# Performance work log

Hardware: AMD Instinct MI355X
Metric: run time of the kernel (lower is better)

## Reference

```python
import jax, jax.numpy as jnp
import numpy as np

TEMPERATURE = 0.07
EPS = 1e-6  # arccosh domain clamp: argument must be >= 1


def setup_inputs() -> dict:
    key = jax.random.key(0)
    k1, k2 = jax.random.split(key)
    N, D = 8192, 768
    v_hyp = jax.random.normal(k1, (N, D), dtype=jnp.float32)
    t_hyp = jax.random.normal(k2, (N, D), dtype=jnp.float32)
    c = jnp.float32(1.0)  # curvature (positive scalar)
    return {"v_hyp": v_hyp, "t_hyp": t_hyp, "c": c}


def _pairwise_hyperbolic_dist(v, t, c):
    # Lorentz/hyperboloid pairwise distance with curvature c:
    #   x_time = sqrt(1/c + ||x||^2)
    #   <x,y>_L = x . y - x_time * y_time
    #   d(x,y) = (1/sqrt(c)) * arccosh(clamp(-c * <x,y>_L, min=1+eps))
    inv_c = 1.0 / c
    v_time = jnp.sqrt(inv_c + jnp.sum(v * v, axis=-1))  # [N]
    t_time = jnp.sqrt(inv_c + jnp.sum(t * t, axis=-1))  # [N]
    lorentz = jnp.einsum("nd,md->nm", v, t) - v_time[:, None] * t_time[None, :]
    arg = jnp.maximum(-c * lorentz, 1.0 + EPS)
    return jnp.sqrt(inv_c) * jnp.arccosh(arg)  # [N, N]


def _ce_diag(logits):
    # cross-entropy with labels = arange(N), mean reduction
    logp = jax.nn.log_softmax(logits, axis=-1)
    return -jnp.mean(jnp.diagonal(logp))


def reference(v_hyp, t_hyp, c):
    dist = _pairwise_hyperbolic_dist(v_hyp, t_hyp, c)
    logits = -dist / TEMPERATURE  # [N, N]
    loss_v2t = _ce_diag(logits)
    loss_t2v = _ce_diag(logits.T)
    return (loss_v2t + loss_t2v) * 0.5
```

## Files before the change

### kernel.cpp

```cpp
#include <hip/hip_runtime.h>
#include <hip/hip_bf16.h>
#include <math.h>

#define NROWS 8192
#define DDIM  768
#define TEMP_INV 14.285714285714286f
#define EPSX 1e-6f
#define NKT  12
#define SHIFT 55.0f
#define QS   20.0f
#define SLOT 24576

typedef __attribute__((ext_vector_type(4))) int   i32x4;
typedef unsigned int   u32;

#define GLOAD16(gaddr, laddr)                                                   \
  __builtin_amdgcn_global_load_lds(                                             \
      (const __attribute__((address_space(1))) u32*)(gaddr),                    \
      (__attribute__((address_space(3))) u32*)(laddr), 16, 0, 0)

#define MFMAI8(a,b,c) __builtin_amdgcn_mfma_i32_16x16x64_i8((a),(b),(c),0,0,0)

__device__ __forceinline__ int q8(float x){
  int q = __float2int_rn(x * QS);
  q = q < -127 ? -127 : (q > 127 ? 127 : q);
  return q & 255;
}

__global__ __launch_bounds__(256) void prep_kernel(
    const float* __restrict__ v, const float* __restrict__ t, const float* __restrict__ cptr,
    u32* __restrict__ vb, u32* __restrict__ tb,
    float* __restrict__ vtime, float* __restrict__ ttime, float* __restrict__ diag)
{
  const int row  = blockIdx.x * 4 + (threadIdx.x >> 6);
  const int lane = threadIdx.x & 63;
  const float inv_c = 1.0f / cptr[0];
  const float4* vr = (const float4*)(v + (size_t)row * DDIM);
  const float4* tr = (const float4*)(t + (size_t)row * DDIM);
  u32* vbr = vb + (size_t)row * (DDIM/4);
  u32* tbr = tb + (size_t)row * (DDIM/4);
  float sv = 0.f, st = 0.f, dd = 0.f;
  #pragma unroll
  for (int it = 0; it < 3; it++){
    int k = lane + it*64;
    float4 a = vr[k], b = tr[k];
    sv += a.x*a.x + a.y*a.y + a.z*a.z + a.w*a.w;
    st += b.x*b.x + b.y*b.y + b.z*b.z + b.w*b.w;
    dd += a.x*b.x + a.y*b.y + a.z*b.z + a.w*b.w;
    vbr[k] = (u32)q8(a.x) | ((u32)q8(a.y)<<8) | ((u32)q8(a.z)<<16) | ((u32)q8(a.w)<<24);
    tbr[k] = (u32)q8(b.x) | ((u32)q8(b.y)<<8) | ((u32)q8(b.z)<<16) | ((u32)q8(b.w)<<24);
  }
  #pragma unroll
  for (int o = 32; o; o >>= 1){
    sv += __shfl_down(sv, o);
    st += __shfl_down(st, o);
    dd += __shfl_down(dd, o);
  }
  if (!lane){
    vtime[row] = sqrtf(inv_c + sv);
    ttime[row] = sqrtf(inv_c + st);
    diag[row]  = dd;
  }
}

__global__ __launch_bounds__(512, 4) void tile_kernel(
    const char* __restrict__ vb, const char* __restrict__ tb,
    const float* __restrict__ vtime, const float* __restrict__ ttime,
    const float* __restrict__ cptr,
    float* __restrict__ rowPsum, float* __restrict__ colPsum)
{
  __shared__ char SMc[3*SLOT];
  __shared__ float vtl2[128], ttl[256];

  const int tid = threadIdx.x;
  const int lane = tid & 63, wid = tid >> 6;
  const int wm = wid >> 2, wn = wid & 3;
  const int lo = lane & 15, hi = lane >> 4;

  const float c = cptr[0];
  const float c2 = c + c;
  const float slog = -(1.0f/sqrtf(c)) * TEMP_INV;
  const float wmin = c2 * (1.0f + EPSX);
  const float kq   = c2 * (1.0f/(QS*QS));

  const int linear = blockIdx.x;
  const int xcd = linear & 7, s = linear >> 3;
  const int xr = xcd & 1, xc = xcd >> 1;
  const int by = xr*32 + (s & 3) + ((s >> 5) << 2);
  const int bx = xc*8 + ((s >> 2) & 7);

  if (tid < 128) vtl2[tid] = c2 * vtime[by*128 + tid];
  if (tid < 256) ttl[tid]  = ttime[bx*256 + tid];

  const char* Abase = vb + (size_t)(by*128) * DDIM;
  const char* Bbase = tb + (size_t)(bx*256) * DDIM;

  const int sx = (tid >> 3) & 3;
  const char* pA  = Abase + (size_t)(tid >> 2)*DDIM        + ((tid & 3) ^ sx)*16;
  const char* pB0 = Bbase + (size_t)(tid >> 2)*DDIM        + ((tid & 3) ^ sx)*16;
  const char* pB1 = Bbase + (size_t)(128 + (tid >> 2))*DDIM + ((tid & 3) ^ sx)*16;
  const int dA  = wid*1024;
  const int dB0 = 8192 + wid*1024;
  const int dB1 = 16384 + wid*1024;

  const int swb  = (hi ^ ((lo >> 1) & 3)) * 16;
  const int arow = (wm*64 + lo) * 64 + swb;
  const int brow = 8192 + (wn*64 + lo) * 64 + swb;

  i32x4 acc[4][4];
  #pragma unroll
  for (int m = 0; m < 4; m++)
    #pragma unroll
    for (int n = 0; n < 4; n++)
      acc[m][n] = (i32x4){0,0,0,0};

#define STG(kt) do{                                                              \
    char* s_ = SMc + ((kt) % 3) * SLOT;                                          \
    GLOAD16(pA  + (kt)*64, s_ + dA);                                             \
    GLOAD16(pB0 + (kt)*64, s_ + dB0);                                            \
    GLOAD16(pB1 + (kt)*64, s_ + dB1); }while(0)

  STG(0); STG(1);
  asm volatile("s_waitcnt vmcnt(3) lgkmcnt(0)" ::: "memory");
  __builtin_amdgcn_s_barrier();

  #pragma unroll
  for (int t = 0; t < NKT; t++){
    __builtin_amdgcn_sched_barrier(0);
    const char* S = SMc + (t % 3) * SLOT;
    if (t + 2 < NKT) STG(t + 2);
    i32x4 b[4];
    #pragma unroll
    for (int n = 0; n < 4; n++) b[n] = *(const i32x4*)(S + brow + n*1024);
    i32x4 a0 = *(const i32x4*)(S + arow);
    i32x4 a1 = *(const i32x4*)(S + arow + 1024);
    i32x4 a2 = *(const i32x4*)(S + arow + 2048);
    i32x4 a3 = *(const i32x4*)(S + arow + 3072);
    __builtin_amdgcn_s_setprio(1);
    #pragma unroll
    for (int n = 0; n < 4; n++){
      acc[0][n] = MFMAI8(a0, b[n], acc[0][n]);
      acc[1][n] = MFMAI8(a1, b[n], acc[1][n]);
      acc[2][n] = MFMAI8(a2, b[n], acc[2][n]);
      acc[3][n] = MFMAI8(a3, b[n], acc[3][n]);
    }
    __builtin_amdgcn_s_setprio(0);
    if (t < NKT-2)       asm volatile("s_waitcnt vmcnt(3) lgkmcnt(0)" ::: "memory");
    else if (t == NKT-2) asm volatile("s_waitcnt vmcnt(0) lgkmcnt(0)" ::: "memory");
    else                 asm volatile("s_waitcnt lgkmcnt(0)" ::: "memory");
    __builtin_amdgcn_s_barrier();
  }
#undef STG

  __syncthreads();

  #pragma unroll
  for (int m = 0; m < 4; m++){
    #pragma unroll
    for (int n = 0; n < 4; n++){
      #pragma unroll
      for (int q = 0; q < 4; q++){
        int r  = wm*64 + m*16 + hi*4 + q;
        int cc = wn*64 + n*16 + lo;
        float w = fmaf(-kq, (float)acc[m][n][q], vtl2[r] * ttl[cc]);
        w = fmaxf(w, wmin);
        acc[m][n][q] = __float_as_int(__expf(fmaf(slog, __logf(w), SHIFT)));
      }
    }
  }

  float* reds  = (float*)SMc;
  float* redcs = reds + 512;

  #pragma unroll
  for (int m = 0; m < 4; m++){
    #pragma unroll
    for (int q = 0; q < 4; q++){
      float s2 = (__int_as_float(acc[m][0][q]) + __int_as_float(acc[m][1][q]))
               + (__int_as_float(acc[m][2][q]) + __int_as_float(acc[m][3][q]));
      #pragma unroll
      for (int msk = 1; msk < 16; msk <<= 1) s2 += __shfl_xor(s2, msk);
      if (lo == 0)
        reds[wn*128 + wm*64 + m*16 + hi*4 + q] = s2;
    }
  }
  __syncthreads();
  if (tid < 128){
    float S = (reds[tid] + reds[128 + tid]) + (reds[256 + tid] + reds[384 + tid]);
    rowPsum[(size_t)bx*NROWS + by*128 + tid] = S;
  }

  #pragma unroll
  for (int n = 0; n < 4; n++){
    float s2 = 0.f;
    #pragma unroll
    for (int m = 0; m < 4; m++)
      #pragma unroll
      for (int q = 0; q < 4; q++) s2 += __int_as_float(acc[m][n][q]);
    s2 += __shfl_xor(s2, 16);
    s2 += __shfl_xor(s2, 32);
    if (hi == 0)
      redcs[wm*256 + wn*64 + n*16 + lo] = s2;
  }
  __syncthreads();
  if (tid < 256){
    float S = redcs[tid] + redcs[256 + tid];
    colPsum[(size_t)by*NROWS + bx*256 + tid] = S;
  }
}

__global__ __launch_bounds__(256) void lse_reduce(
    const float* __restrict__ rowPsum, const float* __restrict__ colPsum,
    float* __restrict__ psums)
{
  const int i = blockIdx.x * 256 + threadIdx.x;
  const float* Ps = blockIdx.y ? colPsum : rowPsum;
  const int nb = blockIdx.y ? 64 : 32;
  float S = 0.f;
  for (int b = 0; b < nb; b++)
    S += Ps[(size_t)b*NROWS + i];
  float lse = __logf(S) - SHIFT;
  for (int o = 32; o; o >>= 1) lse += __shfl_down(lse, o);
  __shared__ float red[4];
  int lane = threadIdx.x & 63, wid = threadIdx.x >> 6;
  if (!lane) red[wid] = lse;
  __syncthreads();
  if (!threadIdx.x)
    psums[blockIdx.y*32 + blockIdx.x] = red[0]+red[1]+red[2]+red[3];
}

__global__ __launch_bounds__(1024) void final_kernel(
    const float* __restrict__ psums, const float* __restrict__ vtime,
    const float* __restrict__ ttime, const float* __restrict__ diag,
    const float* __restrict__ cptr, float* __restrict__ out)
{
  int tid = threadIdx.x;
  float c = cptr[0];
  float slog = -(1.0f/sqrtf(c)) * TEMP_INV;
  float dsum = 0.f;
  #pragma unroll
  for (int it = 0; it < 8; it++){
    int i = tid + it*1024;
    float arg = c * (vtime[i]*ttime[i] - diag[i]);
    arg = fmaxf(arg, 1.0f + EPSX);
    dsum += slog * __logf(arg + sqrtf(arg*arg - 1.0f));
  }
  for (int o = 32; o; o >>= 1) dsum += __shfl_down(dsum, o);
  __shared__ float red[16];
  if (!(tid & 63)) red[tid >> 6] = dsum;
  __syncthreads();
  if (tid < 64){
    float p = psums[tid];
    for (int o = 32; o; o >>= 1) p += __shfl_down(p, o);
    if (!tid){
      float dtot = 0.f;
      #pragma unroll
      for (int k = 0; k < 16; k++) dtot += red[k];
      out[0] = 0.5f*p/NROWS - dtot/NROWS;
    }
  }
}

extern "C" void kernel_launch(void* const* d_in, const int* in_sizes, int n_in,
                              void* d_out, int out_size, void* d_ws, size_t ws_size,
                              hipStream_t stream) {
  const float* v = (const float*)d_in[0];
  const float* t = (const float*)d_in[1];
  const float* c = (const float*)d_in[2];

  char* ws = (char*)d_ws;
  const size_t NB = (size_t)NROWS * DDIM;
  char*  vb      = ws;
  char*  tb      = ws + NB;
  float* vtime   = (float*)(ws + 2*NB);
  float* ttime   = (float*)(ws + 2*NB + NROWS*4);
  float* diag    = (float*)(ws + 2*NB + 2*(size_t)NROWS*4);
  char*  p       = ws + 2*NB + 3*(size_t)NROWS*4;
  float* rowPsum = (float*)(p);
  float* colPsum = (float*)(p + (size_t)32*NROWS*4);
  float* psums   = (float*)(p + (size_t)96*NROWS*4);

  prep_kernel<<<2048, 256, 0, stream>>>(v, t, c, (u32*)vb, (u32*)tb, vtime, ttime, diag);
  tile_kernel<<<2048, 512, 0, stream>>>(vb, tb, vtime, ttime, c, rowPsum, colPsum);
  lse_reduce<<<dim3(32, 2), 256, 0, stream>>>(rowPsum, colPsum, psums);
  final_kernel<<<1, 1024, 0, stream>>>(psums, vtime, ttime, diag, c, (float*)d_out);
}
```

Measured before the change: 114.9 us.

## Shrink tile to 128x128 with 2x4 wave grid to raise occupancy

The tile kernel's output tile drops from 128x256 to 128x128. The grid doubles to 4096 blocks, the LDS slots shrink, each wave holds 2x4 MFMA accumulators instead of 4x4, and launch bounds target 6 blocks per CU. The XCD block mapping, row/column partial-sum layouts and the LSE reduction counts are updated to match. The epilogue now uses exp2/log2 with a pre-scaled shift constant. The smaller tile lowers register and LDS pressure and improves load balance, but it reduces data reuse per block and doubles global reads of the A operand and the partial-sum traffic.

Measured after the change: 102.2 us. 1.12x faster.

```diff
diff --git a/kernel.cpp b/kernel.cpp
--- a/kernel.cpp
+++ b/kernel.cpp
@@ -8,8 +8,9 @@
 #define EPSX 1e-6f
 #define NKT  12
 #define SHIFT 55.0f
+#define SHIFT_E 79.34282475f
 #define QS   20.0f
-#define SLOT 24576
+#define SLOT 16384
 
 typedef __attribute__((ext_vector_type(4))) int   i32x4;
 typedef unsigned int   u32;
@@ -21,10 +22,10 @@
 
 #define MFMAI8(a,b,c) __builtin_amdgcn_mfma_i32_16x16x64_i8((a),(b),(c),0,0,0)
 
-__device__ __forceinline__ int q8(float x){
+__device__ __forceinline__ u32 q8(float x){
   int q = __float2int_rn(x * QS);
   q = q < -127 ? -127 : (q > 127 ? 127 : q);
-  return q & 255;
+  return (u32)(q & 255);
 }
 
 __global__ __launch_bounds__(256) void prep_kernel(
@@ -47,8 +48,8 @@
     sv += a.x*a.x + a.y*a.y + a.z*a.z + a.w*a.w;
     st += b.x*b.x + b.y*b.y + b.z*b.z + b.w*b.w;
     dd += a.x*b.x + a.y*b.y + a.z*b.z + a.w*b.w;
-    vbr[k] = (u32)q8(a.x) | ((u32)q8(a.y)<<8) | ((u32)q8(a.z)<<16) | ((u32)q8(a.w)<<24);
-    tbr[k] = (u32)q8(b.x) | ((u32)q8(b.y)<<8) | ((u32)q8(b.z)<<16) | ((u32)q8(b.w)<<24);
+    vbr[k] = q8(a.x) | (q8(a.y)<<8) | (q8(a.z)<<16) | (q8(a.w)<<24);
+    tbr[k] = q8(b.x) | (q8(b.y)<<8) | (q8(b.z)<<16) | (q8(b.w)<<24);
   }
   #pragma unroll
   for (int o = 32; o; o >>= 1){
@@ -63,18 +64,18 @@
   }
 }
 
-__global__ __launch_bounds__(512, 4) void tile_kernel(
+__global__ __launch_bounds__(512, 6) void tile_kernel(
     const char* __restrict__ vb, const char* __restrict__ tb,
     const float* __restrict__ vtime, const float* __restrict__ ttime,
     const float* __restrict__ cptr,
     float* __restrict__ rowPsum, float* __restrict__ colPsum)
 {
   __shared__ char SMc[3*SLOT];
-  __shared__ float vtl2[128], ttl[256];
+  __shared__ float vtl2[128], ttl[128];
 
   const int tid = threadIdx.x;
   const int lane = tid & 63, wid = tid >> 6;
-  const int wm = wid >> 2, wn = wid & 3;
+  const int wm = wid >> 1, wn = wid & 1;
   const int lo = lane & 15, hi = lane >> 4;
 
   const float c = cptr[0];
@@ -86,42 +87,39 @@
   const int linear = blockIdx.x;
   const int xcd = linear & 7, s = linear >> 3;
   const int xr = xcd & 1, xc = xcd >> 1;
-  const int by = xr*32 + (s & 3) + ((s >> 5) << 2);
-  const int bx = xc*8 + ((s >> 2) & 7);
-
-  if (tid < 128) vtl2[tid] = c2 * vtime[by*128 + tid];
-  if (tid < 256) ttl[tid]  = ttime[bx*256 + tid];
+  const int by = xr*32 + (s & 3) + ((s >> 6) << 2);
+  const int bx = xc*16 + ((s >> 2) & 15);
+
+  if (tid < 128){ vtl2[tid] = c2 * vtime[by*128 + tid]; }
+  else if (tid < 256){ ttl[tid-128] = ttime[bx*128 + tid - 128]; }
 
   const char* Abase = vb + (size_t)(by*128) * DDIM;
-  const char* Bbase = tb + (size_t)(bx*256) * DDIM;
+  const char* Bbase = tb + (size_t)(bx*128) * DDIM;
 
   const int sx = (tid >> 3) & 3;
-  const char* pA  = Abase + (size_t)(tid >> 2)*DDIM        + ((tid & 3) ^ sx)*16;
-  const char* pB0 = Bbase + (size_t)(tid >> 2)*DDIM        + ((tid & 3) ^ sx)*16;
-  const char* pB1 = Bbase + (size_t)(128 + (tid >> 2))*DDIM + ((tid & 3) ^ sx)*16;
-  const int dA  = wid*1024;
-  const int dB0 = 8192 + wid*1024;
-  const int dB1 = 16384 + wid*1024;
+  const char* pA = Abase + (size_t)(tid >> 2)*DDIM + ((tid & 3) ^ sx)*16;
+  const char* pB = Bbase + (size_t)(tid >> 2)*DDIM + ((tid & 3) ^ sx)*16;
+  const int dA = wid*1024;
+  const int dB = 8192 + wid*1024;
 
   const int swb  = (hi ^ ((lo >> 1) & 3)) * 16;
-  const int arow = (wm*64 + lo) * 64 + swb;
+  const int arow = (wm*32 + lo) * 64 + swb;
   const int brow = 8192 + (wn*64 + lo) * 64 + swb;
 
-  i32x4 acc[4][4];
-  #pragma unroll
-  for (int m = 0; m < 4; m++)
+  i32x4 acc[2][4];
+  #pragma unroll
+  for (int m = 0; m < 2; m++)
     #pragma unroll
     for (int n = 0; n < 4; n++)
       acc[m][n] = (i32x4){0,0,0,0};
 
 #define STG(kt) do{                                                              \
     char* s_ = SMc + ((kt) % 3) * SLOT;                                          \
-    GLOAD16(pA  + (kt)*64, s_ + dA);                                             \
-    GLOAD16(pB0 + (kt)*64, s_ + dB0);                                            \
-    GLOAD16(pB1 + (kt)*64, s_ + dB1); }while(0)
+    GLOAD16(pA + (kt)*64, s_ + dA);                                              \
+    GLOAD16(pB + (kt)*64, s_ + dB); }while(0)
 
   STG(0); STG(1);
-  asm volatile("s_waitcnt vmcnt(3) lgkmcnt(0)" ::: "memory");
+  asm volatile("s_waitcnt vmcnt(2) lgkmcnt(0)" ::: "memory");
   __builtin_amdgcn_s_barrier();
 
   #pragma unroll
@@ -134,18 +132,14 @@
     for (int n = 0; n < 4; n++) b[n] = *(const i32x4*)(S + brow + n*1024);
     i32x4 a0 = *(const i32x4*)(S + arow);
     i32x4 a1 = *(const i32x4*)(S + arow + 1024);
-    i32x4 a2 = *(const i32x4*)(S + arow + 2048);
-    i32x4 a3 = *(const i32x4*)(S + arow + 3072);
     __builtin_amdgcn_s_setprio(1);
     #pragma unroll
     for (int n = 0; n < 4; n++){
       acc[0][n] = MFMAI8(a0, b[n], acc[0][n]);
       acc[1][n] = MFMAI8(a1, b[n], acc[1][n]);
-      acc[2][n] = MFMAI8(a2, b[n], acc[2][n]);
-      acc[3][n] = MFMAI8(a3, b[n], acc[3][n]);
     }
     __builtin_amdgcn_s_setprio(0);
-    if (t < NKT-2)       asm volatile("s_waitcnt vmcnt(3) lgkmcnt(0)" ::: "memory");
+    if (t < NKT-2)       asm volatile("s_waitcnt vmcnt(2) lgkmcnt(0)" ::: "memory");
     else if (t == NKT-2) asm volatile("s_waitcnt vmcnt(0) lgkmcnt(0)" ::: "memory");
     else                 asm volatile("s_waitcnt lgkmcnt(0)" ::: "memory");
     __builtin_amdgcn_s_barrier();
@@ -155,25 +149,25 @@
   __syncthreads();
 
   #pragma unroll
-  for (int m = 0; m < 4; m++){
+  for (int m = 0; m < 2; m++){
     #pragma unroll
     for (int n = 0; n < 4; n++){
       #pragma unroll
       for (int q = 0; q < 4; q++){
-        int r  = wm*64 + m*16 + hi*4 + q;
+        int r  = wm*32 + m*16 + hi*4 + q;
         int cc = wn*64 + n*16 + lo;
         float w = fmaf(-kq, (float)acc[m][n][q], vtl2[r] * ttl[cc]);
         w = fmaxf(w, wmin);
-        acc[m][n][q] = __float_as_int(__expf(fmaf(slog, __logf(w), SHIFT)));
+        acc[m][n][q] = __float_as_int(exp2f(fmaf(slog, log2f(w), SHIFT_E)));
       }
     }
   }
 
   float* reds  = (float*)SMc;
-  float* redcs = reds + 512;
-
-  #pragma unroll
-  for (int m = 0; m < 4; m++){
+  float* redcs = reds + 256;
+
+  #pragma unroll
+  for (int m = 0; m < 2; m++){
     #pragma unroll
     for (int q = 0; q < 4; q++){
       float s2 = (__int_as_float(acc[m][0][q]) + __int_as_float(acc[m][1][q]))
@@ -181,12 +175,12 @@
       #pragma unroll
       for (int msk = 1; msk < 16; msk <<= 1) s2 += __shfl_xor(s2, msk);
       if (lo == 0)
-        reds[wn*128 + wm*64 + m*16 + hi*4 + q] = s2;
+        reds[wn*128 + wm*32 + m*16 + hi*4 + q] = s2;
     }
   }
   __syncthreads();
   if (tid < 128){
-    float S = (reds[tid] + reds[128 + tid]) + (reds[256 + tid] + reds[384 + tid]);
+    float S = reds[tid] + reds[128 + tid];
     rowPsum[(size_t)bx*NROWS + by*128 + tid] = S;
   }
 
@@ -194,18 +188,18 @@
   for (int n = 0; n < 4; n++){
     float s2 = 0.f;
     #pragma unroll
-    for (int m = 0; m < 4; m++)
+    for (int m = 0; m < 2; m++)
       #pragma unroll
       for (int q = 0; q < 4; q++) s2 += __int_as_float(acc[m][n][q]);
     s2 += __shfl_xor(s2, 16);
     s2 += __shfl_xor(s2, 32);
     if (hi == 0)
-      redcs[wm*256 + wn*64 + n*16 + lo] = s2;
-  }
-  __syncthreads();
-  if (tid < 256){
-    float S = redcs[tid] + redcs[256 + tid];
-    colPsum[(size_t)by*NROWS + bx*256 + tid] = S;
+      redcs[wm*128 + wn*64 + n*16 + lo] = s2;
+  }
+  __syncthreads();
+  if (tid < 128){
+    float S = (redcs[tid] + redcs[128 + tid]) + (redcs[256 + tid] + redcs[384 + tid]);
+    colPsum[(size_t)by*NROWS + bx*128 + tid] = S;
   }
 }
 
@@ -215,9 +209,8 @@
 {
   const int i = blockIdx.x * 256 + threadIdx.x;
   const float* Ps = blockIdx.y ? colPsum : rowPsum;
-  const int nb = blockIdx.y ? 64 : 32;
   float S = 0.f;
-  for (int b = 0; b < nb; b++)
+  for (int b = 0; b < 64; b++)
     S += Ps[(size_t)b*NROWS + i];
   float lse = __logf(S) - SHIFT;
   for (int o = 32; o; o >>= 1) lse += __shfl_down(lse, o);
@@ -277,11 +270,11 @@
   float* diag    = (float*)(ws + 2*NB + 2*(size_t)NROWS*4);
   char*  p       = ws + 2*NB + 3*(size_t)NROWS*4;
   float* rowPsum = (float*)(p);
-  float* colPsum = (float*)(p + (size_t)32*NROWS*4);
-  float* psums   = (float*)(p + (size_t)96*NROWS*4);
+  float* colPsum = (float*)(p + (size_t)64*NROWS*4);
+  float* psums   = (float*)(p + (size_t)128*NROWS*4);
 
   prep_kernel<<<2048, 256, 0, stream>>>(v, t, c, (u32*)vb, (u32*)tb, vtime, ttime, diag);
-  tile_kernel<<<2048, 512, 0, stream>>>(vb, tb, vtime, ttime, c, rowPsum, colPsum);
+  tile_kernel<<<4096, 512, 0, stream>>>(vb, tb, vtime, ttime, c, rowPsum, colPsum);
   lse_reduce<<<dim3(32, 2), 256, 0, stream>>>(rowPsum, colPsum, psums);
   final_kernel<<<1, 1024, 0, stream>>>(psums, vtime, ttime, diag, c, (float*)d_out);
 }
```
